# Kernel optimization log

Measured on AMD Instinct MI355X. Metric: run time of the kernel, lower is better.

## Reference

```python
import jax, jax.numpy as jnp
import numpy as np

B, T, E, VD, H = 1, 4096, 1024, 2048, 8
KD, HD = E // H, VD // H
EPS = 1e-6


def _make_rel_pos():
    # rotary angles: theta_i = 10000^(-2i/KD), repeated for even/odd pairs
    inv = 1.0 / (10000.0 ** (np.arange(0, KD, 2) / KD))
    angle = np.repeat(inv, 2)[None, :] * np.arange(T)[:, None]  # [T, KD]
    sin = jnp.asarray(np.sin(angle), dtype=jnp.float32)
    cos = jnp.asarray(np.cos(angle), dtype=jnp.float32)
    # per-head causal decay mask: gamma_h^(n-m) for n>=m else 0
    gamma = 1.0 - 2.0 ** (-5.0 - np.arange(H))  # [H]
    n = np.arange(T)
    diff = n[:, None] - n[None, :]  # [T, T]
    logg = np.log(gamma)[:, None, None]
    mask = np.where(diff[None] >= 0, np.exp(logg * np.maximum(diff[None], 0)), 0.0)
    return sin, cos, jnp.asarray(mask, dtype=jnp.float32)


def setup_inputs() -> dict:
    key = jax.random.key(0)
    ks = jax.random.split(key, 6)
    sin, cos, inner_mask = _make_rel_pos()
    s = lambda d: 1.0 / np.sqrt(d)
    return {
        "x": jax.random.normal(ks[0], (B, T, E), dtype=jnp.float32),
        "sin": sin,
        "cos": cos,
        "inner_mask": inner_mask,
        "Wq": jax.random.normal(ks[1], (E, E), dtype=jnp.float32) * s(E),
        "Wk": jax.random.normal(ks[2], (E, E), dtype=jnp.float32) * s(E),
        "Wv": jax.random.normal(ks[3], (E, VD), dtype=jnp.float32) * s(E),
        "Wg": jax.random.normal(ks[4], (E, VD), dtype=jnp.float32) * s(E),
        "Wo": jax.random.normal(ks[5], (VD, E), dtype=jnp.float32) * s(VD),
    }


def _rotate_every_two(x):
    x1 = x[..., ::2]
    x2 = x[..., 1::2]
    return jnp.stack((-x2, x1), axis=-1).reshape(x.shape)


def _theta_shift(x, sin, cos):
    return x * cos + _rotate_every_two(x) * sin


def reference(x, sin, cos, inner_mask, Wq, Wk, Wv, Wg, Wo):
    b, t, e = x.shape
    scaling = KD ** (-0.5)
    q = (x @ Wq).reshape(b, t, H, KD).transpose(0, 2, 1, 3)   # [b,h,t,kd]
    k = (x @ Wk * scaling).reshape(b, t, H, KD).transpose(0, 2, 1, 3)
    v = x @ Wv                                                # [b,t,vd]
    g = x @ Wg                                                # [b,t,vd]
    qr = _theta_shift(q, sin, cos)
    kr = _theta_shift(k, sin, cos)
    vr = v.reshape(b, t, H, HD).transpose(0, 2, 1, 3)         # [b,h,t,hd]
    qk = jnp.einsum('bhtd,bhsd->bhts', qr, kr) * inner_mask   # [b,h,t,t]
    denom = jnp.clip(jnp.abs(jax.lax.stop_gradient(qk)).sum(-1, keepdims=True), 1.0, 50000.0)
    qk = qk / denom
    out = jnp.einsum('bhts,bhsd->bhtd', qk, vr)               # [b,h,t,hd]
    out = out.transpose(0, 2, 1, 3)                           # [b,t,h,hd]
    # RMSNorm over head_dim, no affine
    out = out * jax.lax.rsqrt(jnp.mean(out * out, axis=-1, keepdims=True) + EPS)
    out = out.reshape(b, t, H * HD)
    out = jax.nn.silu(g) * out
    return out @ Wo
```

## Files before the change

kernel.cpp:

```cpp
#include <hip/hip_runtime.h>


typedef __attribute__((ext_vector_type(8)))  short  short8;
typedef __attribute__((ext_vector_type(16))) float  floatx16;

__device__ inline unsigned short f2bf(float f){
  unsigned int u = __builtin_bit_cast(unsigned int, f);
  unsigned int r = (u + 0x7fffu + ((u >> 16) & 1u)) >> 16;
  return (unsigned short)r;
}
__device__ inline float bf2f(unsigned short u){
  unsigned int x = ((unsigned int)u) << 16;
  return __builtin_bit_cast(float, x);
}
__device__ inline void async_cp16(const void* g, const void* l){
  __builtin_amdgcn_global_load_lds((const __attribute__((address_space(1))) void*)g,
                                   (__attribute__((address_space(3))) void*)l, 16, 0, 0);
}

struct us4 { unsigned short a,b,c,d; };
__global__ void k_cvt_x(const float* __restrict__ x, unsigned short* __restrict__ xb, int n4){
  int i = blockIdx.x*blockDim.x + threadIdx.x;
  if (i >= n4) return;
  float4 v = ((const float4*)x)[i];
  us4 o = { f2bf(v.x), f2bf(v.y), f2bf(v.z), f2bf(v.w) };
  ((us4*)xb)[i] = o;
}

struct WPrep  { const float* src; unsigned short* dst; int R; int C; int ntile; };
struct WPrepAll { WPrep w[5]; };
__global__ __launch_bounds__(256) void k_prep_w(WPrepAll a){
  __shared__ float tile[64][65];
  int b = blockIdx.x, i = 0;
  while (b >= a.w[i].ntile){ b -= a.w[i].ntile; ++i; }
  const float* src = a.w[i].src; unsigned short* dst = a.w[i].dst;
  int R = a.w[i].R, C = a.w[i].C;
  int tpr = C >> 6;
  int c0 = (b % tpr)*64, r0 = (b / tpr)*64;
  #pragma unroll
  for (int j=0;j<16;++j){
    int idx = j*256 + threadIdx.x; int r = idx>>6, c = idx&63;
    tile[r][c] = src[(size_t)(r0+r)*C + c0 + c];
  }
  __syncthreads();
  #pragma unroll
  for (int j=0;j<16;++j){
    int idx = j*256 + threadIdx.x; int r = idx>>6, c = idx&63;
    dst[(size_t)(c0+r)*R + r0 + c] = f2bf(tile[c][r]);
  }
}

__global__ __launch_bounds__(256) void k_transpose_b2b(const unsigned short* __restrict__ src,
    unsigned short* __restrict__ dst, int R, int C){
  __shared__ unsigned short tile[64][72];
  int c0 = blockIdx.x*64, r0 = blockIdx.y*64;
  #pragma unroll
  for (int i=0;i<16;++i){
    int idx = i*256 + threadIdx.x; int r = idx>>6, c = idx&63;
    tile[r][c] = src[(size_t)(r0+r)*C + c0 + c];
  }
  __syncthreads();
  #pragma unroll
  for (int i=0;i<16;++i){
    int idx = i*256 + threadIdx.x; int r = idx>>6, c = idx&63;
    dst[(size_t)(c0+r)*R + r0 + c] = tile[c][r];
  }
}

template<int MODE>
__global__ __launch_bounds__(256) void k_gemm_bt(
    const unsigned short* __restrict__ A, const unsigned short* __restrict__ BT,
    int M, int N, int K,
    float* __restrict__ out_f32, unsigned short* __restrict__ out_v,
    unsigned short* __restrict__ out_g)
{
  __shared__ __align__(16) short As[128*64];
  __shared__ __align__(16) short Bs[128*64];
  int bn = blockIdx.x*128, bm = blockIdx.y*128;
  int tid = threadIdx.x;
  int w = tid>>6, l = tid&63;
  int wr = w>>1, wc = w&1;
  int lrow = l&31, lhi = l>>5;
  floatx16 acc[2][2];
  #pragma unroll
  for (int a=0;a<2;++a)
    #pragma unroll
    for (int b=0;b<2;++b)
      #pragma unroll
      for (int j=0;j<16;++j) acc[a][b][j]=0.f;

  int kchunk = K / gridDim.z;
  int k_beg = blockIdx.z * kchunk;
  for (int k0=k_beg; k0<k_beg+kchunk; k0+=64){
    __syncthreads();
    #pragma unroll
    for (int i=0;i<4;++i){
      int idx = i*256 + tid; int r = idx>>3, c = idx&7;
      int cs = c ^ (r&7);
      async_cp16((const char*)A  + ((size_t)(bm+r)*K + k0 + cs*8)*2, &As[idx*8]);
      async_cp16((const char*)BT + ((size_t)(bn+r)*K + k0 + cs*8)*2, &Bs[idx*8]);
    }
    __syncthreads();
    #pragma unroll
    for (int kc=0;kc<4;++kc){
      short8 af[2], bf[2];
      #pragma unroll
      for (int tm=0;tm<2;++tm){
        int row = wr*64 + tm*32 + lrow;
        int pos = (2*kc + lhi) ^ (row&7);
        af[tm] = *(const short8*)&As[row*64 + pos*8];
      }
      #pragma unroll
      for (int tn=0;tn<2;++tn){
        int row = wc*64 + tn*32 + lrow;
        int pos = (2*kc + lhi) ^ (row&7);
        bf[tn] = *(const short8*)&Bs[row*64 + pos*8];
      }
      #pragma unroll
      for (int tm=0;tm<2;++tm)
        #pragma unroll
        for (int tn=0;tn<2;++tn)
          acc[tm][tn] = __builtin_amdgcn_mfma_f32_32x32x16_bf16(af[tm], bf[tn], acc[tm][tn], 0,0,0);
    }
  }
  #pragma unroll
  for (int tm=0;tm<2;++tm)
    #pragma unroll
    for (int tn=0;tn<2;++tn)
      #pragma unroll
      for (int r=0;r<16;++r){
        int row = bm + wr*64 + tm*32 + (r&3) + 8*(r>>2) + 4*lhi;
        int col = bn + wc*64 + tn*32 + lrow;
        float v = acc[tm][tn][r];
        if (MODE==0){
          if (col < 2048)      out_f32[(size_t)row*2048 + col] = v;
          else if (col < 4096) out_v[(size_t)row*2048 + (col-2048)] = f2bf(v);
          else                 out_g[(size_t)row*2048 + (col-4096)] = f2bf(v);
        } else {
          out_f32[(size_t)row*N + col] = v;
        }
      }
}

__global__ void k_rotary(const float* __restrict__ qk, const float* __restrict__ sinp,
                         const float* __restrict__ cosp,
                         unsigned short* __restrict__ qrp, unsigned short* __restrict__ krp)
{
  int tid = blockIdx.x*blockDim.x + threadIdx.x;
  int t = tid >> 10, p = tid & 1023;
  bool isq = p < 512;
  int c = (isq ? p : p - 512)*2;
  int d = c & 127;
  const float* base = qk + (size_t)t*2048 + (isq ? 0 : 1024) + c;
  float f0 = base[0], f1 = base[1];
  float s0 = sinp[t*128 + d],   s1 = sinp[t*128 + d + 1];
  float c0 = cosp[t*128 + d],   c1 = cosp[t*128 + d + 1];
  float r0 = f0*c0 - f1*s0;
  float r1 = f1*c1 + f0*s1;
  if (!isq){ r0 *= 0.08838834764831845f; r1 *= 0.08838834764831845f; }
  unsigned short* dst = (isq ? qrp : krp) + (size_t)t*1024 + c;
  dst[0] = f2bf(r0); dst[1] = f2bf(r1);
}

__global__ __launch_bounds__(256, 2) void k_attn(
    const unsigned short* __restrict__ qr, const unsigned short* __restrict__ kr,
    const unsigned short* __restrict__ vT,
    unsigned short* __restrict__ o_parts, float* __restrict__ den_g)
{
  int gid = blockIdx.x;
  int head = gid & 7;
  int rest = gid >> 3;
  int qt = 63 - (rest >> 2);
  int chunk = rest & 3;
  int tid = threadIdx.x;
  int w = tid>>6, l = tid&63;
  int qh = w>>1, hh = w&1;
  int lrow = l&31, lhi = l>>5;
  int tbase = qt*64 + qh*32;

  float gamma = 1.f - exp2f(-5.f - (float)head);
  float L = log2f(gamma);

  int dmax = (int)(40.0f/(-L));
  int s_start = tbase - dmax; if (s_start < 0) s_start = 0; s_start &= ~31;
  int N = ((tbase - s_start) >> 5) + 1;
  int q4 = (N+3)>>2;
  int t0 = chunk*q4;
  int t1 = t0 + q4; if (t1 > N) t1 = N;

  floatx16 o[4];
  #pragma unroll
  for (int i=0;i<4;++i)
    #pragma unroll
    for (int j=0;j<16;++j) o[i][j]=0.f;
  float den_ = 0.f;

  if (t0 < t1){
    int sb = s_start + t0*32;
    int se = s_start + (t1-1)*32;

    short8 qf[8];
    const unsigned short* qbase = qr + (size_t)(tbase+lrow)*1024 + head*128 + lhi*8;
    #pragma unroll
    for (int kc=0;kc<8;++kc) qf[kc] = *(const short8*)(qbase + kc*16);

    float lanefac = exp2f(L*((float)lrow - 4.0f*(float)lhi));
    float e1[4], e2[4];
    #pragma unroll
    for (int i=0;i<4;++i){ e1[i] = exp2f(-L*(float)i); e2[i] = exp2f(-L*8.0f*(float)i); }

    const unsigned short* kb = kr + head*128 + lhi*8;
    const unsigned short* vb = vT + (size_t)(head*256 + hh*128)*4096 + lhi*8;

#define LOADK(S0, KF) do{ \
    const unsigned short* kp_ = kb + (size_t)((S0)+lrow)*1024; \
    _Pragma("unroll") \
    for (int kc=0;kc<8;++kc) KF[kc] = *(const short8*)(kp_ + kc*16); \
  }while(0)

#define LOADV(S0, VF) do{ \
    const unsigned short* vp_ = vb + (S0); \
    _Pragma("unroll") \
    for (int nt=0;nt<4;++nt){ \
      const unsigned short* vr_ = vp_ + (size_t)(nt*32+lrow)*4096; \
      _Pragma("unroll") \
      for (int kc=0;kc<2;++kc) VF[nt*2+kc] = *(const short8*)(vr_ + kc*16); \
    } \
  }while(0)

#define COMPUTE(S0, KF, VF) do{ \
    floatx16 sa_, sb_; \
    _Pragma("unroll") for (int j=0;j<16;++j){ sa_[j]=0.f; sb_[j]=0.f; } \
    __builtin_amdgcn_s_setprio(1); \
    _Pragma("unroll") \
    for (int kc=0;kc<4;++kc){ \
      sa_ = __builtin_amdgcn_mfma_f32_32x32x16_bf16(KF[kc],   qf[kc],   sa_, 0,0,0); \
      sb_ = __builtin_amdgcn_mfma_f32_32x32x16_bf16(KF[kc+4], qf[kc+4], sb_, 0,0,0); \
    } \
    __builtin_amdgcn_s_setprio(0); \
    float tf_ = exp2f(L*(float)(tbase - (S0))) * lanefac; \
    bool diag_ = ((S0) == tbase); \
    float pv_[16]; \
    _Pragma("unroll") \
    for (int r=0;r<16;++r){ \
      float val_ = (sa_[r]+sb_[r])*(tf_*e1[r&3]*e2[r>>2]); \
      if (diag_){ if (lrow < (r&3)+8*(r>>2)+4*lhi) val_ = 0.f; } \
      den_ += fabsf(val_); \
      pv_[r] = val_; \
    } \
    unsigned int w0_,w1_,w2_,w3_,w4_,w5_,w6_,w7_; \
    asm("v_cvt_pk_bf16_f32 %0, %1, %2" : "=v"(w0_) : "v"(pv_[0]),  "v"(pv_[1])); \
    asm("v_cvt_pk_bf16_f32 %0, %1, %2" : "=v"(w1_) : "v"(pv_[2]),  "v"(pv_[3])); \
    asm("v_cvt_pk_bf16_f32 %0, %1, %2" : "=v"(w2_) : "v"(pv_[4]),  "v"(pv_[5])); \
    asm("v_cvt_pk_bf16_f32 %0, %1, %2" : "=v"(w3_) : "v"(pv_[6]),  "v"(pv_[7])); \
    asm("v_cvt_pk_bf16_f32 %0, %1, %2" : "=v"(w4_) : "v"(pv_[8]),  "v"(pv_[9])); \
    asm("v_cvt_pk_bf16_f32 %0, %1, %2" : "=v"(w5_) : "v"(pv_[10]), "v"(pv_[11])); \
    asm("v_cvt_pk_bf16_f32 %0, %1, %2" : "=v"(w6_) : "v"(pv_[12]), "v"(pv_[13])); \
    asm("v_cvt_pk_bf16_f32 %0, %1, %2" : "=v"(w7_) : "v"(pv_[14]), "v"(pv_[15])); \
    asm("v_permlane32_swap_b32 %0, %1" : "+v"(w0_), "+v"(w2_)); \
    asm("v_permlane32_swap_b32 %0, %1" : "+v"(w1_), "+v"(w3_)); \
    asm("v_permlane32_swap_b32 %0, %1" : "+v"(w4_), "+v"(w6_)); \
    asm("v_permlane32_swap_b32 %0, %1" : "+v"(w5_), "+v"(w7_)); \
    union { unsigned int u[4]; short8 s; } pa0_, pa1_; \
    pa0_.u[0]=w0_; pa0_.u[1]=w1_; pa0_.u[2]=w2_; pa0_.u[3]=w3_; \
    pa1_.u[0]=w4_; pa1_.u[1]=w5_; pa1_.u[2]=w6_; pa1_.u[3]=w7_; \
    __builtin_amdgcn_s_setprio(1); \
    _Pragma("unroll") \
    for (int nt=0;nt<4;++nt){ \
      o[nt] = __builtin_amdgcn_mfma_f32_32x32x16_bf16(pa0_.s, VF[nt*2+0], o[nt], 0,0,0); \
      o[nt] = __builtin_amdgcn_mfma_f32_32x32x16_bf16(pa1_.s, VF[nt*2+1], o[nt], 0,0,0); \
    } \
    __builtin_amdgcn_s_setprio(0); \
  }while(0)

    short8 kfA[8], kfB[8];
    LOADK(sb, kfA);
    for (int s0 = sb;; s0 += 64){
      {
        short8 vfA[8];
        LOADV(s0, vfA);
        if (s0 + 32 <= se) LOADK(s0+32, kfB);
        __builtin_amdgcn_sched_barrier(0);
        COMPUTE(s0, kfA, vfA);
      }
      if (s0 + 32 > se) break;
      {
        short8 vfB[8];
        LOADV(s0+32, vfB);
        if (s0 + 64 <= se) LOADK(s0+64, kfA);
        __builtin_amdgcn_sched_barrier(0);
        COMPUTE(s0+32, kfB, vfB);
      }
      if (s0 + 64 > se) break;
    }
#undef LOADK
#undef LOADV
#undef COMPUTE
  }

  if (hh == 0){
    float d = den_ + __shfl_xor(den_, 32, 64);
    if (lhi == 0)
      den_g[((size_t)chunk*4096 + tbase + lrow)*8 + head] = d;
  }

  unsigned short* ob = o_parts + (size_t)chunk*4096*2048;
  #pragma unroll
  for (int nt=0;nt<4;++nt)
    #pragma unroll
    for (int r=0;r<16;++r){
      int row = (r&3)+8*(r>>2)+4*lhi;
      ob[(size_t)(tbase+row)*2048 + head*256 + hh*128 + nt*32 + lrow] = f2bf(o[nt][r]);
    }
}

__global__ __launch_bounds__(256) void k_rmsgate(const unsigned short* __restrict__ o_parts,
    const unsigned short* __restrict__ g_bf, const float* __restrict__ den_g,
    unsigned short* __restrict__ gated)
{
  int t = blockIdx.x;
  int tid = threadIdx.x;
  int head = tid >> 5;
  float den = den_g[(size_t)t*8 + head]
            + den_g[(size_t)( 4096 + t)*8 + head]
            + den_g[(size_t)( 8192 + t)*8 + head]
            + den_g[(size_t)(12288 + t)*8 + head];
  float rs  = 1.0f/fminf(fmaxf(den, 1.0f), 50000.0f);
  size_t base = (size_t)t*2048 + tid*8;
  const size_t CS = (size_t)4096*2048;
  short8 a0 = *(const short8*)(o_parts + base);
  short8 a1 = *(const short8*)(o_parts + CS + base);
  short8 a2 = *(const short8*)(o_parts + 2*CS + base);
  short8 a3 = *(const short8*)(o_parts + 3*CS + base);
  short8 gv = *(const short8*)(g_bf + base);
  float of[8]; float ss = 0.f;
  #pragma unroll
  for (int j=0;j<8;++j){
    of[j] = (bf2f((unsigned short)a0[j]) + bf2f((unsigned short)a1[j])
           + bf2f((unsigned short)a2[j]) + bf2f((unsigned short)a3[j])) * rs;
    ss += of[j]*of[j];
  }
  #pragma unroll
  for (int off=1; off<32; off<<=1) ss += __shfl_xor(ss, off, 64);
  float rms = rsqrtf(ss*(1.0f/256.0f) + 1e-6f);
  short8 outv;
  #pragma unroll
  for (int j=0;j<8;++j){
    float g = bf2f((unsigned short)gv[j]);
    float si = g / (1.0f + expf(-g));
    outv[j] = (short)f2bf(si * of[j] * rms);
  }
  *(short8*)(gated + base) = outv;
}

extern "C" void kernel_launch(void* const* d_in, const int* in_sizes, int n_in,
                              void* d_out, int out_size, void* d_ws, size_t ws_size,
                              hipStream_t stream)
{
  const float* x    = (const float*)d_in[0];
  const float* sinp = (const float*)d_in[1];
  const float* cosp = (const float*)d_in[2];
  const float* Wq = (const float*)d_in[4];
  const float* Wk = (const float*)d_in[5];
  const float* Wv = (const float*)d_in[6];
  const float* Wg = (const float*)d_in[7];
  const float* Wo = (const float*)d_in[8];

  char* ws = (char*)d_ws;
  size_t off = 0;
  auto alloc = [&](size_t bytes)->char*{ char* p = ws + off; off += (bytes + 255) & ~(size_t)255; return p; };
  unsigned short* x_bf   = (unsigned short*)alloc((size_t)4096*1024*2);
  unsigned short* WallT  = (unsigned short*)alloc((size_t)6144*1024*2);
  float*          qk_f32 = (float*)         alloc((size_t)4096*2048*4);
  unsigned short* v_bf   = (unsigned short*)alloc((size_t)4096*2048*2);
  unsigned short* g_bf   = (unsigned short*)alloc((size_t)4096*2048*2);
  unsigned short* vT     = (unsigned short*)alloc((size_t)2048*4096*2);
  unsigned short* WoT    = (unsigned short*)alloc((size_t)1024*2048*2);
  unsigned short* o_parts= (unsigned short*)alloc((size_t)4*4096*2048*2);
  float*          den_g  = (float*)         alloc((size_t)4*4096*8*4);
  unsigned short* qrp    = x_bf;
  unsigned short* krp    = WallT;
  unsigned short* gated  = x_bf;

  k_cvt_x<<<4096, 256, 0, stream>>>(x, x_bf, 4096*1024/4);
  WPrepAll pa;
  pa.w[0] = { Wq, WallT,                        1024, 1024, 256 };
  pa.w[1] = { Wk, WallT + 1024*1024,            1024, 1024, 256 };
  pa.w[2] = { Wv, WallT + 2048*1024,            1024, 2048, 512 };
  pa.w[3] = { Wg, WallT + (size_t)4096*1024,    1024, 2048, 512 };
  pa.w[4] = { Wo, WoT,                          2048, 1024, 512 };
  k_prep_w<<<2048, 256, 0, stream>>>(pa);

  k_gemm_bt<0><<<dim3(48,32,1), 256, 0, stream>>>(x_bf, WallT, 4096, 6144, 1024, qk_f32, v_bf, g_bf);

  k_rotary<<<16384, 256, 0, stream>>>(qk_f32, sinp, cosp, qrp, krp);

  k_transpose_b2b<<<dim3(32,64), 256, 0, stream>>>(v_bf, vT, 4096, 2048);

  k_attn<<<2048, 256, 0, stream>>>(qrp, krp, vT, o_parts, den_g);

  k_rmsgate<<<4096, 256, 0, stream>>>(o_parts, g_bf, den_g, gated);

  k_gemm_bt<1><<<dim3(8,32,1), 256, 0, stream>>>(gated, WoT, 4096, 1024, 2048,
                                                 (float*)d_out, nullptr, nullptr);

  (void)in_sizes; (void)n_in; (void)out_size; (void)ws_size;
}
```

Baseline: 987.4 us.

## Pre-pack K and V into MFMA fragment order for coalesced attention loads

The rotary kernel now writes K in a per-head, per-32-row-tile layout that matches the MFMA operand fragment order. The V transpose kernel is replaced by one that packs V the same way. The attention kernel then loads each K/V fragment as contiguous 16-byte chunks per lane, where it previously used strided row accesses. This should improve global-load coalescing in the attention inner loop. In exchange, the rotary K stores become scattered 2-byte writes and the pack kernel does strided LDS reads.

```diff
diff --git a/kernel.cpp b/kernel.cpp
--- a/kernel.cpp
+++ b/kernel.cpp
@@ -47,23 +47,6 @@
   for (int j=0;j<16;++j){
     int idx = j*256 + threadIdx.x; int r = idx>>6, c = idx&63;
     dst[(size_t)(c0+r)*R + r0 + c] = f2bf(tile[c][r]);
-  }
-}
-
-__global__ __launch_bounds__(256) void k_transpose_b2b(const unsigned short* __restrict__ src,
-    unsigned short* __restrict__ dst, int R, int C){
-  __shared__ unsigned short tile[64][72];
-  int c0 = blockIdx.x*64, r0 = blockIdx.y*64;
-  #pragma unroll
-  for (int i=0;i<16;++i){
-    int idx = i*256 + threadIdx.x; int r = idx>>6, c = idx&63;
-    tile[r][c] = src[(size_t)(r0+r)*C + c0 + c];
-  }
-  __syncthreads();
-  #pragma unroll
-  for (int i=0;i<16;++i){
-    int idx = i*256 + threadIdx.x; int r = idx>>6, c = idx&63;
-    dst[(size_t)(c0+r)*R + r0 + c] = tile[c][r];
   }
 }
 
@@ -144,7 +127,7 @@
 
 __global__ void k_rotary(const float* __restrict__ qk, const float* __restrict__ sinp,
                          const float* __restrict__ cosp,
-                         unsigned short* __restrict__ qrp, unsigned short* __restrict__ krp)
+                         unsigned short* __restrict__ qrp, unsigned short* __restrict__ krP)
 {
   int tid = blockIdx.x*blockDim.x + threadIdx.x;
   int t = tid >> 10, p = tid & 1023;
@@ -157,14 +140,50 @@
   float c0 = cosp[t*128 + d],   c1 = cosp[t*128 + d + 1];
   float r0 = f0*c0 - f1*s0;
   float r1 = f1*c1 + f0*s1;
-  if (!isq){ r0 *= 0.08838834764831845f; r1 *= 0.08838834764831845f; }
-  unsigned short* dst = (isq ? qrp : krp) + (size_t)t*1024 + c;
-  dst[0] = f2bf(r0); dst[1] = f2bf(r1);
+  if (isq){
+    unsigned short* dst = qrp + (size_t)t*1024 + c;
+    dst[0] = f2bf(r0); dst[1] = f2bf(r1);
+  } else {
+    r0 *= 0.08838834764831845f; r1 *= 0.08838834764831845f;
+    int h  = c >> 7;
+    int dd = c & 127;
+    int kc = dd >> 4, rr = dd & 15;
+    int lhi = rr >> 3, j = rr & 7;
+    size_t idx = (((size_t)(h*128 + (t>>5))*8 + kc)*64 + (t&31) + 32*lhi)*8 + j;
+    krP[idx]   = f2bf(r0);
+    krP[idx+1] = f2bf(r1);
+  }
+}
+
+__global__ __launch_bounds__(256) void k_transpose_pack(const unsigned short* __restrict__ src,
+    unsigned short* __restrict__ vP){
+  __shared__ unsigned short tile[64][72];
+  int c0 = blockIdx.x*64, r0 = blockIdx.y*64;
+  #pragma unroll
+  for (int i=0;i<16;++i){
+    int idx = i*256 + threadIdx.x; int r = idx>>6, c = idx&63;
+    tile[r][c] = src[(size_t)(r0+r)*2048 + c0 + c];
+  }
+  __syncthreads();
+  #pragma unroll
+  for (int it=0; it<2; ++it){
+    int idx = it*256 + threadIdx.x;
+    int cc = idx & 63, so = idx >> 6;
+    int C = c0 + cc;
+    int s = r0 + so*8;
+    int h = C>>8, hh = (C>>7)&1, nt = (C>>5)&3, lrow = C&31;
+    int ts = s>>5, s32 = s&31, kc = s32>>4, lhi = (s32>>3)&1;
+    size_t dst8 = ((size_t)((h*2+hh)*128 + ts)*8 + nt*2+kc)*64 + lrow + 32*lhi;
+    short8 v;
+    #pragma unroll
+    for (int k=0;k<8;++k) v[k] = (short)tile[so*8+k][cc];
+    *(short8*)(vP + dst8*8) = v;
+  }
 }
 
 __global__ __launch_bounds__(256, 2) void k_attn(
-    const unsigned short* __restrict__ qr, const unsigned short* __restrict__ kr,
-    const unsigned short* __restrict__ vT,
+    const unsigned short* __restrict__ qr, const unsigned short* __restrict__ krP,
+    const unsigned short* __restrict__ vP,
     unsigned short* __restrict__ o_parts, float* __restrict__ den_g)
 {
   int gid = blockIdx.x;
@@ -209,23 +228,19 @@
     #pragma unroll
     for (int i=0;i<4;++i){ e1[i] = exp2f(-L*(float)i); e2[i] = exp2f(-L*8.0f*(float)i); }
 
-    const unsigned short* kb = kr + head*128 + lhi*8;
-    const unsigned short* vb = vT + (size_t)(head*256 + hh*128)*4096 + lhi*8;
+    const unsigned short* kbP = krP + (size_t)head*128*4096 + l*8;
+    const unsigned short* vbP = vP  + (size_t)(head*2+hh)*128*4096 + l*8;
 
 #define LOADK(S0, KF) do{ \
-    const unsigned short* kp_ = kb + (size_t)((S0)+lrow)*1024; \
+    const unsigned short* kp_ = kbP + (size_t)((S0)>>5)*4096; \
     _Pragma("unroll") \
-    for (int kc=0;kc<8;++kc) KF[kc] = *(const short8*)(kp_ + kc*16); \
+    for (int kc=0;kc<8;++kc) KF[kc] = *(const short8*)(kp_ + kc*512); \
   }while(0)
 
 #define LOADV(S0, VF) do{ \
-    const unsigned short* vp_ = vb + (S0); \
+    const unsigned short* vp_ = vbP + (size_t)((S0)>>5)*4096; \
     _Pragma("unroll") \
-    for (int nt=0;nt<4;++nt){ \
-      const unsigned short* vr_ = vp_ + (size_t)(nt*32+lrow)*4096; \
-      _Pragma("unroll") \
-      for (int kc=0;kc<2;++kc) VF[nt*2+kc] = *(const short8*)(vr_ + kc*16); \
-    } \
+    for (int f=0;f<8;++f) VF[f] = *(const short8*)(vp_ + f*512); \
   }while(0)
 
 #define COMPUTE(S0, KF, VF) do{ \
@@ -374,12 +389,12 @@
   float*          qk_f32 = (float*)         alloc((size_t)4096*2048*4);
   unsigned short* v_bf   = (unsigned short*)alloc((size_t)4096*2048*2);
   unsigned short* g_bf   = (unsigned short*)alloc((size_t)4096*2048*2);
-  unsigned short* vT     = (unsigned short*)alloc((size_t)2048*4096*2);
+  unsigned short* vP     = (unsigned short*)alloc((size_t)2048*4096*2);
   unsigned short* WoT    = (unsigned short*)alloc((size_t)1024*2048*2);
   unsigned short* o_parts= (unsigned short*)alloc((size_t)4*4096*2048*2);
   float*          den_g  = (float*)         alloc((size_t)4*4096*8*4);
   unsigned short* qrp    = x_bf;
-  unsigned short* krp    = WallT;
+  unsigned short* krP    = WallT;
   unsigned short* gated  = x_bf;
 
   k_cvt_x<<<4096, 256, 0, stream>>>(x, x_bf, 4096*1024/4);
@@ -393,11 +408,11 @@
 
   k_gemm_bt<0><<<dim3(48,32,1), 256, 0, stream>>>(x_bf, WallT, 4096, 6144, 1024, qk_f32, v_bf, g_bf);
 
-  k_rotary<<<16384, 256, 0, stream>>>(qk_f32, sinp, cosp, qrp, krp);
-
-  k_transpose_b2b<<<dim3(32,64), 256, 0, stream>>>(v_bf, vT, 4096, 2048);
-
-  k_attn<<<2048, 256, 0, stream>>>(qrp, krp, vT, o_parts, den_g);
+  k_rotary<<<16384, 256, 0, stream>>>(qk_f32, sinp, cosp, qrp, krP);
+
+  k_transpose_pack<<<dim3(32,64), 256, 0, stream>>>(v_bf, vP);
+
+  k_attn<<<2048, 256, 0, stream>>>(qrp, krP, vP, o_parts, den_g);
 
   k_rmsgate<<<4096, 256, 0, stream>>>(o_parts, g_bf, den_g, gated);
 
```

Result: faster. 844.6 us (-14.5%).
